# Kernel tuning notes

Measured on AMD Instinct MI355X. Metric: run time of the kernel, lower is better.

Reference implementation:

```python
import jax, jax.numpy as jnp
import numpy as np

# Static config (matches init_kwargs)
B, C, H, W = 8, 256, 128, 128
K = 8            # window size per spatial dim
S = K // 2       # shift size
HEADS = 8
E = 256          # embedding_dim
HEAD_DIM = E // HEADS
HID = 3 * C      # mlp hidden
L = K * K        # tokens per window
NW = (H // K) * (W // K)  # windows per image
EPS = 1e-5


def _shift_mask_np():
    # Standard Swin shifted-window attention mask: True = masked.
    img = np.zeros((H, W), dtype=np.int32)
    cnt = 0
    for hs in (slice(0, -K), slice(-K, -S), slice(-S, None)):
        for ws in (slice(0, -K), slice(-K, -S), slice(-S, None)):
            img[hs, ws] = cnt
            cnt += 1
    ids = img.reshape(H // K, K, W // K, K).transpose(0, 2, 1, 3).reshape(NW, L)
    return ids[:, :, None] != ids[:, None, :]  # (NW, L, L) bool

SHIFT_MASK = jnp.asarray(_shift_mask_np())  # (NW, L, L)


def _rpe_index_np():
    coords = np.stack(np.meshgrid(np.arange(K), np.arange(K), indexing='ij'), -1).reshape(L, 2)
    rel = coords[:, None, :] - coords[None, :, :] + (K - 1)  # (L, L, 2) in [0, 2K-2]
    return rel[..., 0] * (2 * K - 1) + rel[..., 1]  # (L, L)

RPE_IDX = jnp.asarray(_rpe_index_np())  # (L, L) int


def window_partition(x):
    # (B, C, H, W) -> (B, NW, L, C)
    x = x.reshape(B, C, H // K, K, W // K, K)
    return x.transpose(0, 2, 4, 3, 5, 1).reshape(B, NW, L, C)


def window_unpartition(x):
    # (B, NW, L, C) -> (B, C, H, W)
    x = x.reshape(B, H // K, W // K, K, K, C)
    return x.transpose(0, 5, 1, 3, 2, 4).reshape(B, C, H, W)


def layer_norm(x, g, b):
    m = jnp.mean(x, axis=-1, keepdims=True)
    v = jnp.mean(jnp.square(x - m), axis=-1, keepdims=True)
    return (x - m) * jax.lax.rsqrt(v + EPS) * g + b


def setup_inputs() -> dict:
    key = jax.random.key(0)
    ks = jax.random.split(key, 12)
    sc = 0.02
    return {
        'query': jax.random.normal(ks[0], (B, C, H, W), jnp.float32),
        'w_q': jax.random.normal(ks[1], (E, C), jnp.float32) * sc,
        'b_q': jnp.zeros((E,), jnp.float32),
        'w_k': jax.random.normal(ks[2], (E, C), jnp.float32) * sc,
        'b_k': jnp.zeros((E,), jnp.float32),
        'w_v': jax.random.normal(ks[3], (E, C), jnp.float32) * sc,
        'b_v': jnp.zeros((E,), jnp.float32),
        'w_proj': jax.random.normal(ks[4], (C, E), jnp.float32) * sc,
        'b_proj': jnp.zeros((C,), jnp.float32),
        'gamma_attn': jnp.ones((C,), jnp.float32),
        'beta_attn': jnp.zeros((C,), jnp.float32),
        'w1': jax.random.normal(ks[5], (HID, C), jnp.float32) * sc,
        'b1': jnp.zeros((HID,), jnp.float32),
        'w2': jax.random.normal(ks[6], (C, HID), jnp.float32) * sc,
        'b2': jnp.zeros((C,), jnp.float32),
        'gamma_mlp': jnp.ones((C,), jnp.float32),
        'beta_mlp': jnp.zeros((C,), jnp.float32),
        'rpe_table': jax.random.normal(ks[7], ((2 * K - 1) ** 2, HEADS), jnp.float32) * sc,
    }


def reference(query, w_q, b_q, w_k, b_k, w_v, b_v, w_proj, b_proj,
              gamma_attn, beta_attn, w1, b1, w2, b2, gamma_mlp, beta_mlp,
              rpe_table) -> jnp.ndarray:
    # cyclic shift (shifted=True)
    xs = jnp.roll(query, (-S, -S), axis=(2, 3))
    xw = window_partition(xs)  # (B, NW, L, C)

    # windowed multi-head attention with relative positional bias
    q = (jnp.einsum('bwlc,ec->bwle', xw, w_q) + b_q).reshape(B, NW, L, HEADS, HEAD_DIM)
    k = (jnp.einsum('bwlc,ec->bwle', xw, w_k) + b_k).reshape(B, NW, L, HEADS, HEAD_DIM)
    v = (jnp.einsum('bwlc,ec->bwle', xw, w_v) + b_v).reshape(B, NW, L, HEADS, HEAD_DIM)
    scale = HEAD_DIM ** -0.5
    scores = jnp.einsum('bwqhd,bwkhd->bwhqk', q, k) * scale  # (B, NW, H, L, L)
    bias = rpe_table[RPE_IDX].transpose(2, 0, 1)  # (HEADS, L, L)
    scores = scores + bias
    scores = jnp.where(SHIFT_MASK[None, :, None, :, :], jnp.float32(-1e9), scores)
    attn = jax.nn.softmax(scores, axis=-1)
    ctx = jnp.einsum('bwhqk,bwkhd->bwqhd', attn, v).reshape(B, NW, L, E)
    attn_out = jnp.einsum('bwle,ce->bwlc', ctx, w_proj) + b_proj

    # post-attention norm + residual (dropout/droppath inactive in eval)
    x = layer_norm(attn_out, gamma_attn, beta_attn) + xw

    # MLP (GELU) + norm + residual
    h = jax.nn.gelu(jnp.einsum('bwlc,hc->bwlh', x, w1) + b1)
    mlp_out = jnp.einsum('bwlh,ch->bwlc', h, w2) + b2
    x = layer_norm(mlp_out, gamma_mlp, beta_mlp) + x

    out = window_unpartition(x)  # (B, C, H, W)
    return jnp.roll(out, (S, S), axis=(2, 3))
```

## Files before the change

### kernel.cpp

```cpp
#include <hip/hip_runtime.h>
#include <hip/hip_bf16.h>

typedef __attribute__((ext_vector_type(8))) __bf16 bf16x8;
typedef __attribute__((ext_vector_type(4))) float f32x4;
typedef __hip_bfloat16 bf16_t;

#define MFMA(a, b, c) __builtin_amdgcn_mfma_f32_16x16x32_bf16((a), (b), (c), 0, 0, 0)

constexpr int XS = 264;
constexpr int CS = 72;
constexpr int XBYTES = 64 * XS * 2;
constexpr int QC_OFF = XBYTES;
constexpr int KC_OFF = QC_OFF + 64 * CS * 2;
constexpr int VC_OFF = KC_OFF + 64 * CS * 2;
constexpr int SCR_OFF = XBYTES + XBYTES;
constexpr int RPE_OFF = SCR_OFF + 64 * 8 * 4;
constexpr int SMEM_TOTAL = RPE_OFF + 225 * 8 * 4;

constexpr size_t O_WQ = 0;
constexpr size_t O_BQ = O_WQ + 65536;
constexpr size_t O_WK = O_BQ + 256;
constexpr size_t O_BK = O_WK + 65536;
constexpr size_t O_WV = O_BK + 256;
constexpr size_t O_BV = O_WV + 65536;
constexpr size_t O_WP = O_BV + 256;
constexpr size_t O_BP = O_WP + 65536;
constexpr size_t O_GA = O_BP + 256;
constexpr size_t O_BA = O_GA + 256;
constexpr size_t O_W1 = O_BA + 256;
constexpr size_t O_B1 = O_W1 + 196608;
constexpr size_t O_W2 = O_B1 + 768;
constexpr size_t O_B2 = O_W2 + 196608;
constexpr size_t O_GM = O_B2 + 256;
constexpr size_t O_BM = O_GM + 256;
constexpr size_t O_RPE = O_BM + 256;
constexpr size_t W_TOTAL = O_RPE + 1800;

__device__ __forceinline__ float red16(float v) {
    v += __shfl_xor(v, 1);
    v += __shfl_xor(v, 2);
    v += __shfl_xor(v, 4);
    v += __shfl_xor(v, 8);
    return v;
}
__device__ __forceinline__ unsigned short bfbits(float x) {
    bf16_t b = __float2bfloat16(x);
    unsigned short u;
    __builtin_memcpy(&u, &b, 2);
    return u;
}
__device__ __forceinline__ ushort4 pack4(float a, float b, float c, float d) {
    ushort4 u;
    u.x = bfbits(a); u.y = bfbits(b); u.z = bfbits(c); u.w = bfbits(d);
    return u;
}

template <typename T>
__device__ __forceinline__ bf16x8 ldfrag(const T* p) {
    if constexpr (sizeof(T) == 4) {
        const float4* q = reinterpret_cast<const float4*>(p);
        float4 a = q[0], b = q[1];
        bf16x8 r;
        r[0] = static_cast<__bf16>(a.x); r[1] = static_cast<__bf16>(a.y);
        r[2] = static_cast<__bf16>(a.z); r[3] = static_cast<__bf16>(a.w);
        r[4] = static_cast<__bf16>(b.x); r[5] = static_cast<__bf16>(b.y);
        r[6] = static_cast<__bf16>(b.z); r[7] = static_cast<__bf16>(b.w);
        return r;
    } else {
        return *reinterpret_cast<const bf16x8*>(p);
    }
}
template <typename T>
__device__ __forceinline__ float ld1(const T* p) {
    if constexpr (sizeof(T) == 4) return *reinterpret_cast<const float*>(p);
    else return __bfloat162float(*reinterpret_cast<const bf16_t*>(p));
}

template <typename T, typename WT>
__device__ void swin_body(
    const T* __restrict__ qin,
    const WT* __restrict__ wq, const WT* __restrict__ bq,
    const WT* __restrict__ wk, const WT* __restrict__ bk,
    const WT* __restrict__ wv, const WT* __restrict__ bv,
    const WT* __restrict__ wp, const WT* __restrict__ bp,
    const WT* __restrict__ ga, const WT* __restrict__ ba,
    const WT* __restrict__ w1, const WT* __restrict__ b1,
    const WT* __restrict__ w2, const WT* __restrict__ b2,
    const WT* __restrict__ gm, const WT* __restrict__ bm,
    const WT* __restrict__ rpe,
    float* __restrict__ outp, char* sm)
{
    bf16_t* xb = reinterpret_cast<bf16_t*>(sm);
    unsigned short* xbs = reinterpret_cast<unsigned short*>(sm);
    bf16_t* qcp = reinterpret_cast<bf16_t*>(sm + QC_OFF);
    bf16_t* kcp = reinterpret_cast<bf16_t*>(sm + KC_OFF);
    bf16_t* vcp = reinterpret_cast<bf16_t*>(sm + VC_OFF);
    float*  scr = reinterpret_cast<float*>(sm + SCR_OFF);
    float*  rpl = reinterpret_cast<float*>(sm + RPE_OFF);
    bf16_t* hb  = reinterpret_cast<bf16_t*>(sm + XBYTES);

    const int tid  = threadIdx.x;
    const int wave = tid >> 6;
    const int lane = tid & 63;
    const int quad = lane >> 4;
    const int l15  = lane & 15;
    const int h32  = (wave & 1) * 32;
    const int rw   = (wave >> 1) * 32;
    const int colbase = wave * 64;

    const int sw = ((blockIdx.x & 7) << 8) | (blockIdx.x >> 3);
    const int bi = sw >> 8;
    const int wl = sw & 255;
    const int wh = wl >> 4, ww = wl & 15;

    const T* qbase = qin + (size_t)bi * (256 * 128 * 128);

    for (int u = tid; u < 4096; u += 256) {
        int ch = u >> 4, r = (u >> 1) & 7, hf = u & 1;
        int hs = (wh * 8 + r + 4) & 127;
        int ws = (ww * 8 + hf * 4 + 4) & 127;
        int t0 = r * 8 + hf * 4;
        if constexpr (sizeof(T) == 4) {
            float4 px = *reinterpret_cast<const float4*>(
                reinterpret_cast<const float*>(qbase) + ch * 16384 + hs * 128 + ws);
            xb[(t0 + 0) * XS + ch] = __float2bfloat16(px.x);
            xb[(t0 + 1) * XS + ch] = __float2bfloat16(px.y);
            xb[(t0 + 2) * XS + ch] = __float2bfloat16(px.z);
            xb[(t0 + 3) * XS + ch] = __float2bfloat16(px.w);
        } else {
            ushort4 px = *reinterpret_cast<const ushort4*>(
                reinterpret_cast<const unsigned short*>(qbase) + ch * 16384 + hs * 128 + ws);
            xbs[(t0 + 0) * XS + ch] = px.x;
            xbs[(t0 + 1) * XS + ch] = px.y;
            xbs[(t0 + 2) * XS + ch] = px.z;
            xbs[(t0 + 3) * XS + ch] = px.w;
        }
    }
    for (int u = tid; u < 1800; u += 256)
        rpl[(u & 7) * 225 + (u >> 3)] = ld1(rpe + u);
    __syncthreads();

    const f32x4 zero = {0.f, 0.f, 0.f, 0.f};

    const bool wh15 = (wh == 15), ww15 = (ww == 15);
    int ridx_[2][4][4];
    unsigned int msk_bits = 0;
    for (int mt = 0; mt < 2; ++mt) {
        int qt = rw + mt * 16 + l15;
        int qr = qt >> 3, qc = qt & 7;
        int qid = (wh15 ? (qr < 4 ? 1 : 2) : 0) * 3 + (ww15 ? (qc < 4 ? 1 : 2) : 0);
        for (int nt = 0; nt < 4; ++nt)
            for (int i = 0; i < 4; ++i) {
                int kt = nt * 16 + quad * 4 + i;
                int kr = kt >> 3, kc = kt & 7;
                int kid = (wh15 ? (kr < 4 ? 1 : 2) : 0) * 3 + (ww15 ? (kc < 4 ? 1 : 2) : 0);
                ridx_[mt][nt][i] = (qr - kr + 7) * 15 + (qc - kc + 7);
                if (qid != kid) msk_bits |= 1u << (mt * 16 + nt * 4 + i);
            }
    }

    f32x4 pacc[4][4];
    for (int mt = 0; mt < 4; ++mt) for (int nt = 0; nt < 4; ++nt) pacc[mt][nt] = zero;

    #pragma unroll 1
    for (int p = 0; p < 4; ++p) {
        const int ecb = p * 64;

        bf16x8 wpa[2][4];
        for (int kbi = 0; kbi < 2; ++kbi)
            for (int nt = 0; nt < 4; ++nt)
                wpa[kbi][nt] = ldfrag<WT>(
                    wp + (size_t)(colbase + nt * 16 + l15) * 256 + ecb + kbi * 32 + quad * 8);

        {
            f32x4 qa[4], ka[4], va[4];
            for (int mt = 0; mt < 4; ++mt) { qa[mt] = zero; ka[mt] = zero; va[mt] = zero; }
            const size_t wrow = (size_t)(ecb + wave * 16 + l15) * 256;
            for (int kb = 0; kb < 256; kb += 32) {
                bf16x8 xf[4];
                for (int mt = 0; mt < 4; ++mt)
                    xf[mt] = *reinterpret_cast<const bf16x8*>(
                        xb + (mt * 16 + l15) * XS + kb + quad * 8);
                bf16x8 bqf = ldfrag<WT>(wq + wrow + kb + quad * 8);
                bf16x8 bkf = ldfrag<WT>(wk + wrow + kb + quad * 8);
                bf16x8 bvf = ldfrag<WT>(wv + wrow + kb + quad * 8);
                for (int mt = 0; mt < 4; ++mt) {
                    qa[mt] = MFMA(bqf, xf[mt], qa[mt]);
                    ka[mt] = MFMA(bkf, xf[mt], ka[mt]);
                    va[mt] = MFMA(xf[mt], bvf, va[mt]);
                }
            }
            float bq4[4], bk4[4];
            for (int i = 0; i < 4; ++i) {
                bq4[i] = ld1(bq + ecb + wave * 16 + quad * 4 + i);
                bk4[i] = ld1(bk + ecb + wave * 16 + quad * 4 + i);
            }
            float bbv = ld1(bv + ecb + wave * 16 + l15);
            for (int mt = 0; mt < 4; ++mt) {
                *reinterpret_cast<ushort4*>(qcp + (mt * 16 + l15) * CS + wave * 16 + quad * 4) =
                    pack4(qa[mt][0] + bq4[0], qa[mt][1] + bq4[1],
                          qa[mt][2] + bq4[2], qa[mt][3] + bq4[3]);
                *reinterpret_cast<ushort4*>(kcp + (mt * 16 + l15) * CS + wave * 16 + quad * 4) =
                    pack4(ka[mt][0] + bk4[0], ka[mt][1] + bk4[1],
                          ka[mt][2] + bk4[2], ka[mt][3] + bk4[3]);
                *reinterpret_cast<ushort4*>(vcp + (wave * 16 + l15) * CS + mt * 16 + quad * 4) =
                    pack4(va[mt][0] + bbv, va[mt][1] + bbv,
                          va[mt][2] + bbv, va[mt][3] + bbv);
            }
        }
        __syncthreads();

        f32x4 sacc[2][4];
        {
            bf16x8 bf_q[2], af_k[4];
            for (int mt = 0; mt < 2; ++mt)
                bf_q[mt] = *reinterpret_cast<const bf16x8*>(
                    qcp + (rw + mt * 16 + l15) * CS + h32 + quad * 8);
            for (int nt = 0; nt < 4; ++nt)
                af_k[nt] = *reinterpret_cast<const bf16x8*>(
                    kcp + (nt * 16 + l15) * CS + h32 + quad * 8);
            for (int mt = 0; mt < 2; ++mt)
                for (int nt = 0; nt < 4; ++nt)
                    sacc[mt][nt] = MFMA(af_k[nt], bf_q[mt], zero);
        }
        __syncthreads();

        const float* rph = rpl + (2 * p + (wave & 1)) * 225;
        bf16_t* preg = (wave & 1) ? kcp : qcp;
        for (int mt = 0; mt < 2; ++mt) {
            for (int nt = 0; nt < 4; ++nt)
                for (int i = 0; i < 4; ++i) {
                    float s = sacc[mt][nt][i] * 0.17677669529663687f;
                    s += rph[ridx_[mt][nt][i]];
                    if (msk_bits & (1u << (mt * 16 + nt * 4 + i))) s = -1e9f;
                    sacc[mt][nt][i] = s;
                }
            float m = sacc[mt][0][0];
            for (int nt = 0; nt < 4; ++nt)
                for (int i = 0; i < 4; ++i) m = fmaxf(m, sacc[mt][nt][i]);
            m = fmaxf(m, __shfl_xor(m, 16));
            m = fmaxf(m, __shfl_xor(m, 32));
            float ssum = 0.f;
            for (int nt = 0; nt < 4; ++nt)
                for (int i = 0; i < 4; ++i) {
                    float e = __expf(sacc[mt][nt][i] - m);
                    sacc[mt][nt][i] = e;
                    ssum += e;
                }
            ssum += __shfl_xor(ssum, 16);
            ssum += __shfl_xor(ssum, 32);
            float inv = 1.0f / ssum;
            for (int nt = 0; nt < 4; ++nt)
                *reinterpret_cast<ushort4*>(
                    preg + (rw + mt * 16 + l15) * CS + nt * 16 + quad * 4) =
                    pack4(sacc[mt][nt][0] * inv, sacc[mt][nt][1] * inv,
                          sacc[mt][nt][2] * inv, sacc[mt][nt][3] * inv);
        }

        f32x4 cacc[2][2];
        for (int mt = 0; mt < 2; ++mt) for (int n2 = 0; n2 < 2; ++n2) cacc[mt][n2] = zero;
        for (int kb = 0; kb < 64; kb += 32) {
            bf16x8 bf_p[2], af_v[2];
            for (int mt = 0; mt < 2; ++mt)
                bf_p[mt] = *reinterpret_cast<const bf16x8*>(
                    preg + (rw + mt * 16 + l15) * CS + kb + quad * 8);
            for (int n2 = 0; n2 < 2; ++n2)
                af_v[n2] = *reinterpret_cast<const bf16x8*>(
                    vcp + (h32 + n2 * 16 + l15) * CS + kb + quad * 8);
            for (int mt = 0; mt < 2; ++mt)
                for (int n2 = 0; n2 < 2; ++n2)
                    cacc[mt][n2] = MFMA(af_v[n2], bf_p[mt], cacc[mt][n2]);
        }
        for (int mt = 0; mt < 2; ++mt)
            for (int n2 = 0; n2 < 2; ++n2)
                *reinterpret_cast<ushort4*>(
                    preg + (rw + mt * 16 + l15) * CS + n2 * 16 + quad * 4) =
                    pack4(cacc[mt][n2][0], cacc[mt][n2][1],
                          cacc[mt][n2][2], cacc[mt][n2][3]);
        __syncthreads();

        for (int kbi = 0; kbi < 2; ++kbi) {
            const bf16_t* creg = kbi ? kcp : qcp;
            bf16x8 af[4];
            for (int mt = 0; mt < 4; ++mt)
                af[mt] = *reinterpret_cast<const bf16x8*>(
                    creg + (mt * 16 + l15) * CS + quad * 8);
            for (int mt = 0; mt < 4; ++mt)
                for (int nt = 0; nt < 4; ++nt)
                    pacc[mt][nt] = MFMA(af[mt], wpa[kbi][nt], pacc[mt][nt]);
        }
        __syncthreads();
    }

    auto layernorm_resid = [&](f32x4 (&acc)[4][4], const WT* gamma, const WT* beta) {
        for (int mt = 0; mt < 4; ++mt)
            for (int rg = 0; rg < 4; ++rg) {
                float s = 0.f, sq = 0.f;
                for (int nt = 0; nt < 4; ++nt) {
                    float v = acc[mt][nt][rg];
                    s += v;
                    sq += v * v;
                }
                s = red16(s);
                sq = red16(sq);
                if (l15 == 0) {
                    int tok = mt * 16 + quad * 4 + rg;
                    scr[tok * 8 + wave * 2 + 0] = s;
                    scr[tok * 8 + wave * 2 + 1] = sq;
                }
            }
        __syncthreads();
        for (int mt = 0; mt < 4; ++mt)
            for (int rg = 0; rg < 4; ++rg) {
                int tok = mt * 16 + quad * 4 + rg;
                float S = 0.f, SQ = 0.f;
                for (int w_ = 0; w_ < 4; ++w_) {
                    S += scr[tok * 8 + w_ * 2 + 0];
                    SQ += scr[tok * 8 + w_ * 2 + 1];
                }
                float mean = S * (1.f / 256.f);
                float var = fmaxf(SQ * (1.f / 256.f) - mean * mean, 0.f);
                float rstd = rsqrtf(var + 1e-5f);
                for (int nt = 0; nt < 4; ++nt) {
                    int c = colbase + nt * 16 + l15;
                    float g = ld1(gamma + c);
                    float b_ = ld1(beta + c);
                    float res = __bfloat162float(xb[tok * XS + c]);
                    float o = (acc[mt][nt][rg] - mean) * rstd * g + b_ + res;
                    xb[tok * XS + c] = __float2bfloat16(o);
                }
            }
        __syncthreads();
    };

    {
        for (int nt = 0; nt < 4; ++nt) {
            float bb = ld1(bp + colbase + nt * 16 + l15);
            for (int mt = 0; mt < 4; ++mt)
                for (int rg = 0; rg < 4; ++rg) pacc[mt][nt][rg] += bb;
        }
        layernorm_resid(pacc, ga, ba);
    }

    {
        f32x4 oacc[4][4];
        for (int mt = 0; mt < 4; ++mt) for (int nt = 0; nt < 4; ++nt) oacc[mt][nt] = zero;
        for (int hc = 0; hc < 3; ++hc) {
            f32x4 hacc[4][4];
            for (int nt = 0; nt < 4; ++nt) for (int mt = 0; mt < 4; ++mt) hacc[nt][mt] = zero;
            for (int kb = 0; kb < 256; kb += 32) {
                bf16x8 xf[4], wf[4];
                for (int mt = 0; mt < 4; ++mt)
                    xf[mt] = *reinterpret_cast<const bf16x8*>(
                        xb + (mt * 16 + l15) * XS + kb + quad * 8);
                for (int nt = 0; nt < 4; ++nt)
                    wf[nt] = ldfrag<WT>(
                        w1 + (size_t)(hc * 256 + colbase + nt * 16 + l15) * 256 + kb + quad * 8);
                for (int nt = 0; nt < 4; ++nt)
                    for (int mt = 0; mt < 4; ++mt)
                        hacc[nt][mt] = MFMA(wf[nt], xf[mt], hacc[nt][mt]);
            }
            for (int nt = 0; nt < 4; ++nt) {
                float b4[4];
                for (int i = 0; i < 4; ++i)
                    b4[i] = ld1(b1 + hc * 256 + colbase + nt * 16 + quad * 4 + i);
                for (int mt = 0; mt < 4; ++mt) {
                    float g4[4];
                    for (int i = 0; i < 4; ++i) {
                        float x = hacc[nt][mt][i] + b4[i];
                        float u = 0.7978845608f * (x + 0.044715f * x * x * x);
                        float t = 1.f - 2.f / (1.f + __expf(2.f * u));
                        g4[i] = 0.5f * x * (1.f + t);
                    }
                    *reinterpret_cast<ushort4*>(
                        hb + (mt * 16 + l15) * XS + colbase + nt * 16 + quad * 4) =
                        pack4(g4[0], g4[1], g4[2], g4[3]);
                }
            }
            __syncthreads();
            for (int kb = 0; kb < 256; kb += 32) {
                bf16x8 af[4], bfr[4];
                for (int mt = 0; mt < 4; ++mt)
                    af[mt] = *reinterpret_cast<const bf16x8*>(
                        hb + (mt * 16 + l15) * XS + kb + quad * 8);
                for (int nt = 0; nt < 4; ++nt)
                    bfr[nt] = ldfrag<WT>(
                        w2 + (size_t)(colbase + nt * 16 + l15) * 768 + hc * 256 + kb + quad * 8);
                for (int mt = 0; mt < 4; ++mt)
                    for (int nt = 0; nt < 4; ++nt)
                        oacc[mt][nt] = MFMA(af[mt], bfr[nt], oacc[mt][nt]);
            }
            __syncthreads();
        }
        for (int nt = 0; nt < 4; ++nt) {
            float bb = ld1(b2 + colbase + nt * 16 + l15);
            for (int mt = 0; mt < 4; ++mt)
                for (int rg = 0; rg < 4; ++rg) oacc[mt][nt][rg] += bb;
        }
        layernorm_resid(oacc, gm, bm);
    }

    for (int u = tid; u < 4096; u += 256) {
        int ch = u >> 4, r = (u >> 1) & 7, hf = u & 1;
        int hs = (wh * 8 + r + 4) & 127;
        int ws = (ww * 8 + hf * 4 + 4) & 127;
        int t0 = r * 8 + hf * 4;
        float4 px;
        px.x = __bfloat162float(xb[(t0 + 0) * XS + ch]);
        px.y = __bfloat162float(xb[(t0 + 1) * XS + ch]);
        px.z = __bfloat162float(xb[(t0 + 2) * XS + ch]);
        px.w = __bfloat162float(xb[(t0 + 3) * XS + ch]);
        *reinterpret_cast<float4*>(
            outp + (size_t)bi * 4194304 + ch * 16384 + hs * 128 + ws) = px;
    }
}

__global__ void convert_weights_kernel(
    const void* wq, const void* bq, const void* wk, const void* bk,
    const void* wv, const void* bv, const void* wp, const void* bp,
    const void* ga, const void* ba, const void* w1, const void* b1,
    const void* w2, const void* b2, const void* gm, const void* bm,
    const void* rpe, bf16_t* ws)
{
    if (*reinterpret_cast<const unsigned short*>(ga) == 0x3F80) return;
    const float* srcs[17] = {
        (const float*)wq, (const float*)bq, (const float*)wk, (const float*)bk,
        (const float*)wv, (const float*)bv, (const float*)wp, (const float*)bp,
        (const float*)ga, (const float*)ba, (const float*)w1, (const float*)b1,
        (const float*)w2, (const float*)b2, (const float*)gm, (const float*)bm,
        (const float*)rpe};
    const size_t offs[18] = {O_WQ, O_BQ, O_WK, O_BK, O_WV, O_BV, O_WP, O_BP, O_GA,
                             O_BA, O_W1, O_B1, O_W2, O_B2, O_GM, O_BM, O_RPE, W_TOTAL};
    for (size_t i = blockIdx.x * (size_t)blockDim.x + threadIdx.x; i < W_TOTAL;
         i += (size_t)gridDim.x * blockDim.x) {
        int s = 0;
        while (s < 16 && i >= offs[s + 1]) ++s;
        ws[i] = __float2bfloat16(srcs[s][i - offs[s]]);
    }
}

__global__ __launch_bounds__(256, 2) void swin_block_kernel(
    const void* qin,
    const void* wq, const void* bq, const void* wk, const void* bk,
    const void* wv, const void* bv, const void* wp, const void* bp,
    const void* ga, const void* ba, const void* w1, const void* b1,
    const void* w2, const void* b2, const void* gm, const void* bm,
    const void* rpe, float* outp, const bf16_t* ws, int use_ws)
{
    extern __shared__ char smem[];
    const bool is_bf16 = (*reinterpret_cast<const unsigned short*>(ga) == 0x3F80);
    if (is_bf16) {
        swin_body<bf16_t, bf16_t>((const bf16_t*)qin,
            (const bf16_t*)wq, (const bf16_t*)bq, (const bf16_t*)wk, (const bf16_t*)bk,
            (const bf16_t*)wv, (const bf16_t*)bv, (const bf16_t*)wp, (const bf16_t*)bp,
            (const bf16_t*)ga, (const bf16_t*)ba, (const bf16_t*)w1, (const bf16_t*)b1,
            (const bf16_t*)w2, (const bf16_t*)b2, (const bf16_t*)gm, (const bf16_t*)bm,
            (const bf16_t*)rpe, outp, smem);
    } else if (use_ws) {
        swin_body<float, bf16_t>((const float*)qin,
            ws + O_WQ, ws + O_BQ, ws + O_WK, ws + O_BK, ws + O_WV, ws + O_BV,
            ws + O_WP, ws + O_BP, ws + O_GA, ws + O_BA, ws + O_W1, ws + O_B1,
            ws + O_W2, ws + O_B2, ws + O_GM, ws + O_BM, ws + O_RPE, outp, smem);
    } else {
        swin_body<float, float>((const float*)qin,
            (const float*)wq, (const float*)bq, (const float*)wk, (const float*)bk,
            (const float*)wv, (const float*)bv, (const float*)wp, (const float*)bp,
            (const float*)ga, (const float*)ba, (const float*)w1, (const float*)b1,
            (const float*)w2, (const float*)b2, (const float*)gm, (const float*)bm,
            (const float*)rpe, outp, smem);
    }
}

extern "C" void kernel_launch(void* const* d_in, const int* in_sizes, int n_in,
                              void* d_out, int out_size, void* d_ws, size_t ws_size,
                              hipStream_t stream) {
    (void)in_sizes; (void)n_in; (void)out_size;
    const int use_ws = (d_ws != nullptr && ws_size >= W_TOTAL * sizeof(bf16_t)) ? 1 : 0;
    if (use_ws) {
        convert_weights_kernel<<<256, 256, 0, stream>>>(
            d_in[1], d_in[2], d_in[3], d_in[4], d_in[5], d_in[6], d_in[7], d_in[8],
            d_in[9], d_in[10], d_in[11], d_in[12], d_in[13], d_in[14], d_in[15], d_in[16],
            d_in[17], (bf16_t*)d_ws);
    }
    hipFuncSetAttribute(reinterpret_cast<const void*>(swin_block_kernel),
                        hipFuncAttributeMaxDynamicSharedMemorySize, SMEM_TOTAL);
    swin_block_kernel<<<2048, 256, SMEM_TOTAL, stream>>>(
        d_in[0], d_in[1], d_in[2], d_in[3], d_in[4], d_in[5], d_in[6], d_in[7], d_in[8],
        d_in[9], d_in[10], d_in[11], d_in[12], d_in[13], d_in[14], d_in[15], d_in[16],
        d_in[17], (float*)d_out, (const bf16_t*)d_ws, use_ws);
}
```

Baseline: 797.1 us.

## Shrink shared memory and registers to fit three blocks per CU

```diff
diff --git a/kernel.cpp b/kernel.cpp
--- a/kernel.cpp
+++ b/kernel.cpp
@@ -3,6 +3,7 @@
 
 typedef __attribute__((ext_vector_type(8))) __bf16 bf16x8;
 typedef __attribute__((ext_vector_type(4))) float f32x4;
+typedef __attribute__((ext_vector_type(4))) unsigned int u32x4;
 typedef __hip_bfloat16 bf16_t;
 
 #define MFMA(a, b, c) __builtin_amdgcn_mfma_f32_16x16x32_bf16((a), (b), (c), 0, 0, 0)
@@ -12,10 +13,9 @@
 constexpr int XBYTES = 64 * XS * 2;
 constexpr int QC_OFF = XBYTES;
 constexpr int KC_OFF = QC_OFF + 64 * CS * 2;
-constexpr int VC_OFF = KC_OFF + 64 * CS * 2;
-constexpr int SCR_OFF = XBYTES + XBYTES;
-constexpr int RPE_OFF = SCR_OFF + 64 * 8 * 4;
-constexpr int SMEM_TOTAL = RPE_OFF + 225 * 8 * 4;
+constexpr int HBS = 136;
+constexpr int SCR_OFF = XBYTES + 64 * HBS * 2;
+constexpr int SMEM_TOTAL = SCR_OFF + 64 * 8 * 4;
 
 constexpr size_t O_WQ = 0;
 constexpr size_t O_BQ = O_WQ + 65536;
@@ -54,6 +54,9 @@
     u.x = bfbits(a); u.y = bfbits(b); u.z = bfbits(c); u.w = bfbits(d);
     return u;
 }
+__device__ __forceinline__ unsigned pack2(float lo, float hi) {
+    return (unsigned)bfbits(lo) | ((unsigned)bfbits(hi) << 16);
+}
 
 template <typename T>
 __device__ __forceinline__ bf16x8 ldfrag(const T* p) {
@@ -87,17 +90,15 @@
     const WT* __restrict__ w1, const WT* __restrict__ b1,
     const WT* __restrict__ w2, const WT* __restrict__ b2,
     const WT* __restrict__ gm, const WT* __restrict__ bm,
-    const WT* __restrict__ rpe,
+    const WT* __restrict__ rpe, int rpe_sh, int rpe_sr,
     float* __restrict__ outp, char* sm)
 {
     bf16_t* xb = reinterpret_cast<bf16_t*>(sm);
     unsigned short* xbs = reinterpret_cast<unsigned short*>(sm);
     bf16_t* qcp = reinterpret_cast<bf16_t*>(sm + QC_OFF);
     bf16_t* kcp = reinterpret_cast<bf16_t*>(sm + KC_OFF);
-    bf16_t* vcp = reinterpret_cast<bf16_t*>(sm + VC_OFF);
+    bf16_t* hb  = reinterpret_cast<bf16_t*>(sm + XBYTES);
     float*  scr = reinterpret_cast<float*>(sm + SCR_OFF);
-    float*  rpl = reinterpret_cast<float*>(sm + RPE_OFF);
-    bf16_t* hb  = reinterpret_cast<bf16_t*>(sm + XBYTES);
 
     const int tid  = threadIdx.x;
     const int wave = tid >> 6;
@@ -136,8 +137,6 @@
             xbs[(t0 + 3) * XS + ch] = px.w;
         }
     }
-    for (int u = tid; u < 1800; u += 256)
-        rpl[(u & 7) * 225 + (u >> 3)] = ld1(rpe + u);
     __syncthreads();
 
     const f32x4 zero = {0.f, 0.f, 0.f, 0.f};
@@ -159,23 +158,29 @@
             }
     }
 
+    auto mkbfp = [&](const unsigned (&w)[8], int kbase) -> bf16x8 {
+        u32x4 r;
+        #pragma unroll
+        for (int t = 0; t < 4; ++t) {
+            int srcl = (quad & 1) * 32 + (t >> 1) * 16 + l15;
+            unsigned lo = (unsigned)__shfl((int)w[(kbase >> 3) + (t & 1)], srcl);
+            unsigned hi = (unsigned)__shfl((int)w[(kbase >> 3) + 2 + (t & 1)], srcl);
+            r[t] = (quad & 2) ? hi : lo;
+        }
+        return __builtin_bit_cast(bf16x8, r);
+    };
+
     f32x4 pacc[4][4];
     for (int mt = 0; mt < 4; ++mt) for (int nt = 0; nt < 4; ++nt) pacc[mt][nt] = zero;
 
     #pragma unroll 1
     for (int p = 0; p < 4; ++p) {
         const int ecb = p * 64;
-
-        bf16x8 wpa[2][4];
-        for (int kbi = 0; kbi < 2; ++kbi)
-            for (int nt = 0; nt < 4; ++nt)
-                wpa[kbi][nt] = ldfrag<WT>(
-                    wp + (size_t)(colbase + nt * 16 + l15) * 256 + ecb + kbi * 32 + quad * 8);
+        const size_t wrow = (size_t)(ecb + wave * 16 + l15) * 256;
 
         {
-            f32x4 qa[4], ka[4], va[4];
-            for (int mt = 0; mt < 4; ++mt) { qa[mt] = zero; ka[mt] = zero; va[mt] = zero; }
-            const size_t wrow = (size_t)(ecb + wave * 16 + l15) * 256;
+            f32x4 qa[4], ka[4];
+            for (int mt = 0; mt < 4; ++mt) { qa[mt] = zero; ka[mt] = zero; }
             for (int kb = 0; kb < 256; kb += 32) {
                 bf16x8 xf[4];
                 for (int mt = 0; mt < 4; ++mt)
@@ -183,11 +188,9 @@
                         xb + (mt * 16 + l15) * XS + kb + quad * 8);
                 bf16x8 bqf = ldfrag<WT>(wq + wrow + kb + quad * 8);
                 bf16x8 bkf = ldfrag<WT>(wk + wrow + kb + quad * 8);
-                bf16x8 bvf = ldfrag<WT>(wv + wrow + kb + quad * 8);
                 for (int mt = 0; mt < 4; ++mt) {
                     qa[mt] = MFMA(bqf, xf[mt], qa[mt]);
                     ka[mt] = MFMA(bkf, xf[mt], ka[mt]);
-                    va[mt] = MFMA(xf[mt], bvf, va[mt]);
                 }
             }
             float bq4[4], bk4[4];
@@ -195,7 +198,6 @@
                 bq4[i] = ld1(bq + ecb + wave * 16 + quad * 4 + i);
                 bk4[i] = ld1(bk + ecb + wave * 16 + quad * 4 + i);
             }
-            float bbv = ld1(bv + ecb + wave * 16 + l15);
             for (int mt = 0; mt < 4; ++mt) {
                 *reinterpret_cast<ushort4*>(qcp + (mt * 16 + l15) * CS + wave * 16 + quad * 4) =
                     pack4(qa[mt][0] + bq4[0], qa[mt][1] + bq4[1],
@@ -203,9 +205,6 @@
                 *reinterpret_cast<ushort4*>(kcp + (mt * 16 + l15) * CS + wave * 16 + quad * 4) =
                     pack4(ka[mt][0] + bk4[0], ka[mt][1] + bk4[1],
                           ka[mt][2] + bk4[2], ka[mt][3] + bk4[3]);
-                *reinterpret_cast<ushort4*>(vcp + (wave * 16 + l15) * CS + mt * 16 + quad * 4) =
-                    pack4(va[mt][0] + bbv, va[mt][1] + bbv,
-                          va[mt][2] + bbv, va[mt][3] + bbv);
             }
         }
         __syncthreads();
@@ -225,13 +224,20 @@
         }
         __syncthreads();
 
-        const float* rph = rpl + (2 * p + (wave & 1)) * 225;
-        bf16_t* preg = (wave & 1) ? kcp : qcp;
+        bf16x8 wpa[2][4];
+        for (int kbi = 0; kbi < 2; ++kbi)
+            for (int nt = 0; nt < 4; ++nt)
+                wpa[kbi][nt] = ldfrag<WT>(
+                    wp + (size_t)(colbase + nt * 16 + l15) * 256 + ecb + kbi * 32 + quad * 8);
+
+        const int h = 2 * p + (wave & 1);
+        const WT* rph = rpe + (size_t)h * rpe_sh;
+        unsigned pw[2][8];
         for (int mt = 0; mt < 2; ++mt) {
             for (int nt = 0; nt < 4; ++nt)
                 for (int i = 0; i < 4; ++i) {
                     float s = sacc[mt][nt][i] * 0.17677669529663687f;
-                    s += rph[ridx_[mt][nt][i]];
+                    s += ld1(rph + (size_t)ridx_[mt][nt][i] * rpe_sr);
                     if (msk_bits & (1u << (mt * 16 + nt * 4 + i))) s = -1e9f;
                     sacc[mt][nt][i] = s;
                 }
@@ -251,40 +257,68 @@
             ssum += __shfl_xor(ssum, 32);
             float inv = 1.0f / ssum;
             for (int nt = 0; nt < 4; ++nt)
+                for (int hh = 0; hh < 2; ++hh)
+                    pw[mt][nt * 2 + hh] = pack2(sacc[mt][nt][2 * hh] * inv,
+                                                sacc[mt][nt][2 * hh + 1] * inv);
+        }
+
+        {
+            f32x4 va[4];
+            for (int mt = 0; mt < 4; ++mt) va[mt] = zero;
+            for (int kb = 0; kb < 256; kb += 32) {
+                bf16x8 xf[4];
+                for (int mt = 0; mt < 4; ++mt)
+                    xf[mt] = *reinterpret_cast<const bf16x8*>(
+                        xb + (mt * 16 + l15) * XS + kb + quad * 8);
+                bf16x8 bvf = ldfrag<WT>(wv + wrow + kb + quad * 8);
+                for (int mt = 0; mt < 4; ++mt)
+                    va[mt] = MFMA(xf[mt], bvf, va[mt]);
+            }
+            float bbv = ld1(bv + ecb + wave * 16 + l15);
+            for (int mt = 0; mt < 4; ++mt)
                 *reinterpret_cast<ushort4*>(
-                    preg + (rw + mt * 16 + l15) * CS + nt * 16 + quad * 4) =
-                    pack4(sacc[mt][nt][0] * inv, sacc[mt][nt][1] * inv,
-                          sacc[mt][nt][2] * inv, sacc[mt][nt][3] * inv);
-        }
+                    qcp + (wave * 16 + l15) * CS + mt * 16 + quad * 4) =
+                    pack4(va[mt][0] + bbv, va[mt][1] + bbv,
+                          va[mt][2] + bbv, va[mt][3] + bbv);
+        }
+        __syncthreads();
 
         f32x4 cacc[2][2];
         for (int mt = 0; mt < 2; ++mt) for (int n2 = 0; n2 < 2; ++n2) cacc[mt][n2] = zero;
-        for (int kb = 0; kb < 64; kb += 32) {
-            bf16x8 bf_p[2], af_v[2];
-            for (int mt = 0; mt < 2; ++mt)
-                bf_p[mt] = *reinterpret_cast<const bf16x8*>(
-                    preg + (rw + mt * 16 + l15) * CS + kb + quad * 8);
+        {
+            bf16x8 bp0, bp1, af_v[2];
+            bp0 = mkbfp(pw[0], 0);
+            bp1 = mkbfp(pw[1], 0);
             for (int n2 = 0; n2 < 2; ++n2)
                 af_v[n2] = *reinterpret_cast<const bf16x8*>(
-                    vcp + (h32 + n2 * 16 + l15) * CS + kb + quad * 8);
-            for (int mt = 0; mt < 2; ++mt)
-                for (int n2 = 0; n2 < 2; ++n2)
-                    cacc[mt][n2] = MFMA(af_v[n2], bf_p[mt], cacc[mt][n2]);
+                    qcp + (h32 + n2 * 16 + l15) * CS + 0 + quad * 8);
+            for (int n2 = 0; n2 < 2; ++n2) {
+                cacc[0][n2] = MFMA(af_v[n2], bp0, cacc[0][n2]);
+                cacc[1][n2] = MFMA(af_v[n2], bp1, cacc[1][n2]);
+            }
+            bp0 = mkbfp(pw[0], 32);
+            bp1 = mkbfp(pw[1], 32);
+            for (int n2 = 0; n2 < 2; ++n2)
+                af_v[n2] = *reinterpret_cast<const bf16x8*>(
+                    qcp + (h32 + n2 * 16 + l15) * CS + 32 + quad * 8);
+            for (int n2 = 0; n2 < 2; ++n2) {
+                cacc[0][n2] = MFMA(af_v[n2], bp0, cacc[0][n2]);
+                cacc[1][n2] = MFMA(af_v[n2], bp1, cacc[1][n2]);
+            }
         }
         for (int mt = 0; mt < 2; ++mt)
             for (int n2 = 0; n2 < 2; ++n2)
                 *reinterpret_cast<ushort4*>(
-                    preg + (rw + mt * 16 + l15) * CS + n2 * 16 + quad * 4) =
+                    kcp + (rw + mt * 16 + l15) * CS + h32 + n2 * 16 + quad * 4) =
                     pack4(cacc[mt][n2][0], cacc[mt][n2][1],
                           cacc[mt][n2][2], cacc[mt][n2][3]);
         __syncthreads();
 
         for (int kbi = 0; kbi < 2; ++kbi) {
-            const bf16_t* creg = kbi ? kcp : qcp;
             bf16x8 af[4];
             for (int mt = 0; mt < 4; ++mt)
                 af[mt] = *reinterpret_cast<const bf16x8*>(
-                    creg + (mt * 16 + l15) * CS + quad * 8);
+                    kcp + (mt * 16 + l15) * CS + kbi * 32 + quad * 8);
             for (int mt = 0; mt < 4; ++mt)
                 for (int nt = 0; nt < 4; ++nt)
                     pacc[mt][nt] = MFMA(af[mt], wpa[kbi][nt], pacc[mt][nt]);
@@ -345,25 +379,26 @@
     {
         f32x4 oacc[4][4];
         for (int mt = 0; mt < 4; ++mt) for (int nt = 0; nt < 4; ++nt) oacc[mt][nt] = zero;
-        for (int hc = 0; hc < 3; ++hc) {
-            f32x4 hacc[4][4];
-            for (int nt = 0; nt < 4; ++nt) for (int mt = 0; mt < 4; ++mt) hacc[nt][mt] = zero;
+        #pragma unroll 1
+        for (int hc = 0; hc < 6; ++hc) {
+            f32x4 hacc[2][4];
+            for (int nt = 0; nt < 2; ++nt) for (int mt = 0; mt < 4; ++mt) hacc[nt][mt] = zero;
             for (int kb = 0; kb < 256; kb += 32) {
-                bf16x8 xf[4], wf[4];
+                bf16x8 xf[4], wf[2];
                 for (int mt = 0; mt < 4; ++mt)
                     xf[mt] = *reinterpret_cast<const bf16x8*>(
                         xb + (mt * 16 + l15) * XS + kb + quad * 8);
-                for (int nt = 0; nt < 4; ++nt)
+                for (int nt = 0; nt < 2; ++nt)
                     wf[nt] = ldfrag<WT>(
-                        w1 + (size_t)(hc * 256 + colbase + nt * 16 + l15) * 256 + kb + quad * 8);
-                for (int nt = 0; nt < 4; ++nt)
+                        w1 + (size_t)(hc * 128 + wave * 32 + nt * 16 + l15) * 256 + kb + quad * 8);
+                for (int nt = 0; nt < 2; ++nt)
                     for (int mt = 0; mt < 4; ++mt)
                         hacc[nt][mt] = MFMA(wf[nt], xf[mt], hacc[nt][mt]);
             }
-            for (int nt = 0; nt < 4; ++nt) {
+            for (int nt = 0; nt < 2; ++nt) {
                 float b4[4];
                 for (int i = 0; i < 4; ++i)
-                    b4[i] = ld1(b1 + hc * 256 + colbase + nt * 16 + quad * 4 + i);
+                    b4[i] = ld1(b1 + hc * 128 + wave * 32 + nt * 16 + quad * 4 + i);
                 for (int mt = 0; mt < 4; ++mt) {
                     float g4[4];
                     for (int i = 0; i < 4; ++i) {
@@ -373,19 +408,19 @@
                         g4[i] = 0.5f * x * (1.f + t);
                     }
                     *reinterpret_cast<ushort4*>(
-                        hb + (mt * 16 + l15) * XS + colbase + nt * 16 + quad * 4) =
+                        hb + (mt * 16 + l15) * HBS + wave * 32 + nt * 16 + quad * 4) =
                         pack4(g4[0], g4[1], g4[2], g4[3]);
                 }
             }
             __syncthreads();
-            for (int kb = 0; kb < 256; kb += 32) {
+            for (int kb = 0; kb < 128; kb += 32) {
                 bf16x8 af[4], bfr[4];
                 for (int mt = 0; mt < 4; ++mt)
                     af[mt] = *reinterpret_cast<const bf16x8*>(
-                        hb + (mt * 16 + l15) * XS + kb + quad * 8);
+                        hb + (mt * 16 + l15) * HBS + kb + quad * 8);
                 for (int nt = 0; nt < 4; ++nt)
                     bfr[nt] = ldfrag<WT>(
-                        w2 + (size_t)(colbase + nt * 16 + l15) * 768 + hc * 256 + kb + quad * 8);
+                        w2 + (size_t)(colbase + nt * 16 + l15) * 768 + hc * 128 + kb + quad * 8);
                 for (int mt = 0; mt < 4; ++mt)
                     for (int nt = 0; nt < 4; ++nt)
                         oacc[mt][nt] = MFMA(af[mt], bfr[nt], oacc[mt][nt]);
@@ -435,11 +470,17 @@
          i += (size_t)gridDim.x * blockDim.x) {
         int s = 0;
         while (s < 16 && i >= offs[s + 1]) ++s;
-        ws[i] = __float2bfloat16(srcs[s][i - offs[s]]);
-    }
-}
-
-__global__ __launch_bounds__(256, 2) void swin_block_kernel(
+        bf16_t v = __float2bfloat16(srcs[s][i - offs[s]]);
+        if (s == 16) {
+            size_t local = i - O_RPE;
+            ws[O_RPE + (local & 7) * 225 + (local >> 3)] = v;
+        } else {
+            ws[i] = v;
+        }
+    }
+}
+
+__global__ __launch_bounds__(256, 3) void swin_block_kernel(
     const void* qin,
     const void* wq, const void* bq, const void* wk, const void* bk,
     const void* wv, const void* bv, const void* wp, const void* bp,
@@ -455,19 +496,19 @@
             (const bf16_t*)wv, (const bf16_t*)bv, (const bf16_t*)wp, (const bf16_t*)bp,
             (const bf16_t*)ga, (const bf16_t*)ba, (const bf16_t*)w1, (const bf16_t*)b1,
             (const bf16_t*)w2, (const bf16_t*)b2, (const bf16_t*)gm, (const bf16_t*)bm,
-            (const bf16_t*)rpe, outp, smem);
+            (const bf16_t*)rpe, 1, 8, outp, smem);
     } else if (use_ws) {
         swin_body<float, bf16_t>((const float*)qin,
             ws + O_WQ, ws + O_BQ, ws + O_WK, ws + O_BK, ws + O_WV, ws + O_BV,
             ws + O_WP, ws + O_BP, ws + O_GA, ws + O_BA, ws + O_W1, ws + O_B1,
-            ws + O_W2, ws + O_B2, ws + O_GM, ws + O_BM, ws + O_RPE, outp, smem);
+            ws + O_W2, ws + O_B2, ws + O_GM, ws + O_BM, ws + O_RPE, 225, 1, outp, smem);
     } else {
         swin_body<float, float>((const float*)qin,
             (const float*)wq, (const float*)bq, (const float*)wk, (const float*)bk,
             (const float*)wv, (const float*)bv, (const float*)wp, (const float*)bp,
             (const float*)ga, (const float*)ba, (const float*)w1, (const float*)b1,
             (const float*)w2, (const float*)b2, (const float*)gm, (const float*)bm,
-            (const float*)rpe, outp, smem);
+            (const float*)rpe, 1, 8, outp, smem);
     }
 }
 
```

Result: slower. 954.0 us (+19.7%).

## Prefetch weight fragments one step ahead and raise wave priority around MFMA bursts

Applied to the files above, without the earlier changes.

```diff
diff --git a/kernel.cpp b/kernel.cpp
--- a/kernel.cpp
+++ b/kernel.cpp
@@ -176,19 +176,27 @@
             f32x4 qa[4], ka[4], va[4];
             for (int mt = 0; mt < 4; ++mt) { qa[mt] = zero; ka[mt] = zero; va[mt] = zero; }
             const size_t wrow = (size_t)(ecb + wave * 16 + l15) * 256;
+            bf16x8 bqf = ldfrag<WT>(wq + wrow + quad * 8);
+            bf16x8 bkf = ldfrag<WT>(wk + wrow + quad * 8);
+            bf16x8 bvf = ldfrag<WT>(wv + wrow + quad * 8);
+            #pragma unroll
             for (int kb = 0; kb < 256; kb += 32) {
+                const int kbn = (kb + 32) & 255;
+                bf16x8 nqf = ldfrag<WT>(wq + wrow + kbn + quad * 8);
+                bf16x8 nkf = ldfrag<WT>(wk + wrow + kbn + quad * 8);
+                bf16x8 nvf = ldfrag<WT>(wv + wrow + kbn + quad * 8);
                 bf16x8 xf[4];
                 for (int mt = 0; mt < 4; ++mt)
                     xf[mt] = *reinterpret_cast<const bf16x8*>(
                         xb + (mt * 16 + l15) * XS + kb + quad * 8);
-                bf16x8 bqf = ldfrag<WT>(wq + wrow + kb + quad * 8);
-                bf16x8 bkf = ldfrag<WT>(wk + wrow + kb + quad * 8);
-                bf16x8 bvf = ldfrag<WT>(wv + wrow + kb + quad * 8);
+                __builtin_amdgcn_s_setprio(1);
                 for (int mt = 0; mt < 4; ++mt) {
                     qa[mt] = MFMA(bqf, xf[mt], qa[mt]);
                     ka[mt] = MFMA(bkf, xf[mt], ka[mt]);
                     va[mt] = MFMA(xf[mt], bvf, va[mt]);
                 }
+                __builtin_amdgcn_s_setprio(0);
+                bqf = nqf; bkf = nkf; bvf = nvf;
             }
             float bq4[4], bk4[4];
             for (int i = 0; i < 4; ++i) {
@@ -196,10 +204,11 @@
                 bk4[i] = ld1(bk + ecb + wave * 16 + quad * 4 + i);
             }
             float bbv = ld1(bv + ecb + wave * 16 + l15);
+            const float SC = 0.17677669529663687f;
             for (int mt = 0; mt < 4; ++mt) {
                 *reinterpret_cast<ushort4*>(qcp + (mt * 16 + l15) * CS + wave * 16 + quad * 4) =
-                    pack4(qa[mt][0] + bq4[0], qa[mt][1] + bq4[1],
-                          qa[mt][2] + bq4[2], qa[mt][3] + bq4[3]);
+                    pack4((qa[mt][0] + bq4[0]) * SC, (qa[mt][1] + bq4[1]) * SC,
+                          (qa[mt][2] + bq4[2]) * SC, (qa[mt][3] + bq4[3]) * SC);
                 *reinterpret_cast<ushort4*>(kcp + (mt * 16 + l15) * CS + wave * 16 + quad * 4) =
                     pack4(ka[mt][0] + bk4[0], ka[mt][1] + bk4[1],
                           ka[mt][2] + bk4[2], ka[mt][3] + bk4[3]);
@@ -219,9 +228,11 @@
             for (int nt = 0; nt < 4; ++nt)
                 af_k[nt] = *reinterpret_cast<const bf16x8*>(
                     kcp + (nt * 16 + l15) * CS + h32 + quad * 8);
+            __builtin_amdgcn_s_setprio(1);
             for (int mt = 0; mt < 2; ++mt)
                 for (int nt = 0; nt < 4; ++nt)
                     sacc[mt][nt] = MFMA(af_k[nt], bf_q[mt], zero);
+            __builtin_amdgcn_s_setprio(0);
         }
         __syncthreads();
 
@@ -230,7 +241,7 @@
         for (int mt = 0; mt < 2; ++mt) {
             for (int nt = 0; nt < 4; ++nt)
                 for (int i = 0; i < 4; ++i) {
-                    float s = sacc[mt][nt][i] * 0.17677669529663687f;
+                    float s = sacc[mt][nt][i];
                     s += rph[ridx_[mt][nt][i]];
                     if (msk_bits & (1u << (mt * 16 + nt * 4 + i))) s = -1e9f;
                     sacc[mt][nt][i] = s;
@@ -267,9 +278,11 @@
             for (int n2 = 0; n2 < 2; ++n2)
                 af_v[n2] = *reinterpret_cast<const bf16x8*>(
                     vcp + (h32 + n2 * 16 + l15) * CS + kb + quad * 8);
+            __builtin_amdgcn_s_setprio(1);
             for (int mt = 0; mt < 2; ++mt)
                 for (int n2 = 0; n2 < 2; ++n2)
                     cacc[mt][n2] = MFMA(af_v[n2], bf_p[mt], cacc[mt][n2]);
+            __builtin_amdgcn_s_setprio(0);
         }
         for (int mt = 0; mt < 2; ++mt)
             for (int n2 = 0; n2 < 2; ++n2)
@@ -285,9 +298,11 @@
             for (int mt = 0; mt < 4; ++mt)
                 af[mt] = *reinterpret_cast<const bf16x8*>(
                     creg + (mt * 16 + l15) * CS + quad * 8);
+            __builtin_amdgcn_s_setprio(1);
             for (int mt = 0; mt < 4; ++mt)
                 for (int nt = 0; nt < 4; ++nt)
                     pacc[mt][nt] = MFMA(af[mt], wpa[kbi][nt], pacc[mt][nt]);
+            __builtin_amdgcn_s_setprio(0);
         }
         __syncthreads();
     }
@@ -348,17 +363,28 @@
         for (int hc = 0; hc < 3; ++hc) {
             f32x4 hacc[4][4];
             for (int nt = 0; nt < 4; ++nt) for (int mt = 0; mt < 4; ++mt) hacc[nt][mt] = zero;
-            for (int kb = 0; kb < 256; kb += 32) {
-                bf16x8 xf[4], wf[4];
-                for (int mt = 0; mt < 4; ++mt)
-                    xf[mt] = *reinterpret_cast<const bf16x8*>(
-                        xb + (mt * 16 + l15) * XS + kb + quad * 8);
+            {
+                bf16x8 wf[4], nwf[4];
                 for (int nt = 0; nt < 4; ++nt)
                     wf[nt] = ldfrag<WT>(
-                        w1 + (size_t)(hc * 256 + colbase + nt * 16 + l15) * 256 + kb + quad * 8);
-                for (int nt = 0; nt < 4; ++nt)
+                        w1 + (size_t)(hc * 256 + colbase + nt * 16 + l15) * 256 + quad * 8);
+                #pragma unroll
+                for (int kb = 0; kb < 256; kb += 32) {
+                    const int kbn = (kb + 32) & 255;
+                    for (int nt = 0; nt < 4; ++nt)
+                        nwf[nt] = ldfrag<WT>(
+                            w1 + (size_t)(hc * 256 + colbase + nt * 16 + l15) * 256 + kbn + quad * 8);
+                    bf16x8 xf[4];
                     for (int mt = 0; mt < 4; ++mt)
-                        hacc[nt][mt] = MFMA(wf[nt], xf[mt], hacc[nt][mt]);
+                        xf[mt] = *reinterpret_cast<const bf16x8*>(
+                            xb + (mt * 16 + l15) * XS + kb + quad * 8);
+                    __builtin_amdgcn_s_setprio(1);
+                    for (int nt = 0; nt < 4; ++nt)
+                        for (int mt = 0; mt < 4; ++mt)
+                            hacc[nt][mt] = MFMA(wf[nt], xf[mt], hacc[nt][mt]);
+                    __builtin_amdgcn_s_setprio(0);
+                    for (int nt = 0; nt < 4; ++nt) wf[nt] = nwf[nt];
+                }
             }
             for (int nt = 0; nt < 4; ++nt) {
                 float b4[4];
@@ -378,17 +404,28 @@
                 }
             }
             __syncthreads();
-            for (int kb = 0; kb < 256; kb += 32) {
-                bf16x8 af[4], bfr[4];
-                for (int mt = 0; mt < 4; ++mt)
-                    af[mt] = *reinterpret_cast<const bf16x8*>(
-                        hb + (mt * 16 + l15) * XS + kb + quad * 8);
+            {
+                bf16x8 bfr[4], nbfr[4];
                 for (int nt = 0; nt < 4; ++nt)
                     bfr[nt] = ldfrag<WT>(
-                        w2 + (size_t)(colbase + nt * 16 + l15) * 768 + hc * 256 + kb + quad * 8);
-                for (int mt = 0; mt < 4; ++mt)
+                        w2 + (size_t)(colbase + nt * 16 + l15) * 768 + hc * 256 + quad * 8);
+                #pragma unroll
+                for (int kb = 0; kb < 256; kb += 32) {
+                    const int kbn = (kb + 32) & 255;
                     for (int nt = 0; nt < 4; ++nt)
-                        oacc[mt][nt] = MFMA(af[mt], bfr[nt], oacc[mt][nt]);
+                        nbfr[nt] = ldfrag<WT>(
+                            w2 + (size_t)(colbase + nt * 16 + l15) * 768 + hc * 256 + kbn + quad * 8);
+                    bf16x8 af[4];
+                    for (int mt = 0; mt < 4; ++mt)
+                        af[mt] = *reinterpret_cast<const bf16x8*>(
+                            hb + (mt * 16 + l15) * XS + kb + quad * 8);
+                    __builtin_amdgcn_s_setprio(1);
+                    for (int mt = 0; mt < 4; ++mt)
+                        for (int nt = 0; nt < 4; ++nt)
+                            oacc[mt][nt] = MFMA(af[mt], bfr[nt], oacc[mt][nt]);
+                    __builtin_amdgcn_s_setprio(0);
+                    for (int nt = 0; nt < 4; ++nt) bfr[nt] = nbfr[nt];
+                }
             }
             __syncthreads();
         }
```

New measurement: 789.5 us, median of 2. About the same (-0.9%).
